# Optimization experiments

Measured on AMD Instinct MI355X. Metric: run time of the kernel, lower is better.

The kernel has to match this reference:

```python
import jax, jax.numpy as jnp
import numpy as np

B, D_IN, H, N_LAYERS, D_OUT = 262144, 8, 128, 3, 1


def setup_inputs() -> dict:
    key = jax.random.key(0)
    ks = jax.random.split(key, 18)
    rn = lambda k, shape, fan: (jax.random.normal(k, shape, jnp.float32) / np.sqrt(fan))
    return {
        "x": jax.random.normal(ks[0], (B, D_IN), jnp.float32),
        "Sw_w": rn(ks[1], (D_IN, H), D_IN),
        "Sw_b": rn(ks[2], (H,), D_IN),
        "Uz": rn(ks[3], (N_LAYERS, D_IN, H), D_IN),
        "Wsz_w": rn(ks[4], (N_LAYERS, H, H), H),
        "Wsz_b": rn(ks[5], (N_LAYERS, H), H),
        "Ug": rn(ks[6], (N_LAYERS, D_IN, H), D_IN),
        "Wsg_w": rn(ks[7], (N_LAYERS, H, H), H),
        "Wsg_b": rn(ks[8], (N_LAYERS, H), H),
        "Ur": rn(ks[9], (N_LAYERS, D_IN, H), D_IN),
        "Wsr_w": rn(ks[10], (N_LAYERS, H, H), H),
        "Wsr_b": rn(ks[11], (N_LAYERS, H), H),
        "Uh": rn(ks[12], (N_LAYERS, D_IN, H), D_IN),
        "Wsh_w": rn(ks[13], (N_LAYERS, H, H), H),
        "Wsh_b": rn(ks[14], (N_LAYERS, H), H),
        "Wf_w": rn(ks[15], (H, D_OUT), H),
        "Wf_b": rn(ks[16], (D_OUT,), H),
    }


def reference(x, Sw_w, Sw_b, Uz, Wsz_w, Wsz_b, Ug, Wsg_w, Wsg_b,
              Ur, Wsr_w, Wsr_b, Uh, Wsh_w, Wsh_b, Wf_w, Wf_b):
    # x: [B, D_in]; S: [B, H]
    S = x @ Sw_w + Sw_b
    n = Uz.shape[0]
    for i in range(n):  # small fixed layer count
        S = jax.nn.sigmoid(S)
        Z = jax.nn.sigmoid(x @ Uz[i] + S @ Wsz_w[i] + Wsz_b[i])
        G = jax.nn.sigmoid(x @ Ug[i] + S @ Wsg_w[i] + Wsg_b[i])
        R = jax.nn.sigmoid(x @ Ur[i] + S @ Wsr_w[i] + Wsr_b[i])
        H_ = jnp.tanh(x @ Uh[i] + (S * R) @ Wsh_w[i] + Wsh_b[i])
        S = (1.0 - G) * H_ + Z * S
    return S @ Wf_w + Wf_b  # [B, D_out]
```

## Files before the change

### kernel.cpp

```cpp
#include <hip/hip_runtime.h>

typedef __bf16 bf16_t;
typedef __bf16 bf16x4 __attribute__((ext_vector_type(4)));
typedef __bf16 bf16x8 __attribute__((ext_vector_type(8)));
typedef float f32x4 __attribute__((ext_vector_type(4)));

#define NL 3
#define HD 128
#define ROWS 64
#define SSTR 136
#define RSTR 136
#define XSTR 24
#define THREADS 512
#define BATCH 262144
#define NBLK (BATCH / ROWS)

#define SW_OFF 0
#define U_OFF  4096
#define W_OFF  53248
#define WS_ELEMS 249856

#define MFMA(a, b, c) __builtin_amdgcn_mfma_f32_16x16x32_bf16((a), (b), (c), 0, 0, 0)

#define LOG2E 1.4426950408889634f
__device__ __forceinline__ float sige(float a) {
    return __builtin_amdgcn_rcpf(1.f + __builtin_amdgcn_exp2f(a));
}
__device__ __forceinline__ float tanhe(float a) {
    return 1.f - 2.f * __builtin_amdgcn_rcpf(__builtin_amdgcn_exp2f(a) + 1.f);
}
__device__ __forceinline__ float sigm(float v) {
    return __builtin_amdgcn_rcpf(1.f + __builtin_amdgcn_exp2f(-LOG2E * v));
}

__global__ void dgm_prep(const float* __restrict__ SwW, const float* __restrict__ Swb,
                         const float* __restrict__ Uz, const float* __restrict__ Wz, const float* __restrict__ Bz,
                         const float* __restrict__ Ug, const float* __restrict__ Wg, const float* __restrict__ Bg,
                         const float* __restrict__ Ur, const float* __restrict__ Wr, const float* __restrict__ Br,
                         const float* __restrict__ Uh, const float* __restrict__ Wh,
                         bf16_t* __restrict__ ws) {
    int idx = blockIdx.x * 256 + threadIdx.x;
    if (idx >= WS_ELEMS) return;
    const float* Us[4] = {Uz, Ug, Ur, Uh};
    const float* Wm[4] = {Wz, Wg, Wr, Wh};
    const float gsc[4] = {-LOG2E, LOG2E, -LOG2E, 2.f * LOG2E};
    if (idx < U_OFF) {
        int ct = idx >> 9, rem = idx & 511, lane = rem >> 3, j = rem & 7;
        int q = lane >> 4, mm = lane & 15;
        int k = q * 8 + j, n = ct * 16 + mm;
        float v = (k < 8) ? SwW[k * HD + n] : (k == 8) ? Swb[n] : 0.f;
        ws[idx] = (bf16_t)(v * -LOG2E);
    } else if (idx < W_OFF) {
        int t = idx - U_OFF;
        int lg = t >> 12, r2 = t & 4095;
        int l = lg >> 2, g = lg & 3;
        int ct = r2 >> 9, rem = r2 & 511, lane = rem >> 3, j = rem & 7;
        int q = lane >> 4, mm = lane & 15;
        int k = q * 8 + j, n = ct * 16 + mm;
        const float* Bs = (g == 0) ? Bz : (g == 1) ? Bg : (g == 2) ? Br : (const float*)0;
        float v = (k < 8) ? Us[g][(l * 8 + k) * HD + n]
                : (k == 8 && g < 3) ? Bs[l * HD + n] : 0.f;
        ws[idx] = (bf16_t)(v * gsc[g]);
    } else {
        int t = idx - W_OFF;
        int lg = t >> 14, r2 = t & 16383;
        int l = lg >> 2, g = lg & 3;
        int ct = r2 >> 11, kc = (r2 >> 9) & 3, rem = r2 & 511, lane = rem >> 3, j = rem & 7;
        int q = lane >> 4, mm = lane & 15;
        int k = kc * 32 + q * 8 + j, n = ct * 16 + mm;
        ws[idx] = (bf16_t)(Wm[g][(l * HD + k) * HD + n] * gsc[g]);
    }
}

__global__ __launch_bounds__(THREADS, 4) void dgm_main(
    const float* __restrict__ x,
    const float* __restrict__ Bh,
    const float* __restrict__ WfW, const float* __restrict__ WfB,
    const bf16_t* __restrict__ ws,
    float* __restrict__ out) {
    __shared__ __align__(16) bf16_t s_sig[ROWS * SSTR];
    __shared__ __align__(16) bf16_t s_r[ROWS * RSTR];
    __shared__ __align__(16) bf16_t s_xo[ROWS * XSTR];
    __shared__ float red[ROWS];

    const int tid = threadIdx.x;
    const int lane = tid & 63;
    const int ct = tid >> 6;
    const int m = lane & 15, q = lane >> 4;
    const int rb = blockIdx.x * ROWS;
    const int f0 = ct * 16 + q * 4;
    const int fragoff = (ct * 64 + lane) * 8;
    const int wfragoff = (ct * 4) * 512 + lane * 8;
    const int xoff = (q ? 8 : 0);

    if (tid < ROWS) red[tid] = 0.f;

    {
        int r = tid >> 3, j = tid & 7;
        s_xo[r * XSTR + j] = (bf16_t)x[(size_t)(rb + r) * 8 + j];
        s_xo[r * XSTR + 8 + j] = (j == 0) ? (bf16_t)1.f : (bf16_t)0.f;
    }
    __syncthreads();

    bf16x4 svp[4];

    {
        bf16x8 fSw = *(const bf16x8*)(ws + SW_OFF + fragoff);
#pragma unroll
        for (int bt = 0; bt < 4; bt++) {
            bf16x8 b = *(const bf16x8*)(&s_xo[(bt * 16 + m) * XSTR + xoff]);
            f32x4 acc = {0.f, 0.f, 0.f, 0.f};
            acc = MFMA(fSw, b, acc);
            bf16x4 pk;
#pragma unroll
            for (int i = 0; i < 4; i++) pk[i] = (bf16_t)sige(acc[i]);
            svp[bt] = pk;
            *(bf16x4*)(&s_sig[(bt * 16 + m) * SSTR + f0]) = pk;
        }
    }
    __syncthreads();

#pragma unroll 1
    for (int l = 0; l < NL; l++) {
        const bool last = (l == NL - 1);
        const bf16_t* wb = ws + W_OFF + (size_t)l * 4 * 16384;
        const bf16_t* ub = ws + U_OFF + (size_t)l * 4 * 4096;

        {
            bf16x8 fU = *(const bf16x8*)(ub + 2 * 4096 + fragoff);
            bf16x8 fW[4];
#pragma unroll
            for (int kc = 0; kc < 4; kc++)
                fW[kc] = *(const bf16x8*)(wb + 2 * 16384 + wfragoff + kc * 512);
#pragma unroll
            for (int bt = 0; bt < 4; bt++) {
                const bf16_t* bbase = &s_sig[(bt * 16 + m) * SSTR];
                const bf16_t* xbase = &s_xo[(bt * 16 + m) * XSTR];
                f32x4 aR = {0.f, 0.f, 0.f, 0.f};
#pragma unroll
                for (int kc = 0; kc < 4; kc++) {
                    bf16x8 b = *(const bf16x8*)(bbase + kc * 32 + q * 8);
                    aR = MFMA(fW[kc], b, aR);
                }
                {
                    bf16x8 b = *(const bf16x8*)(xbase + xoff);
                    aR = MFMA(fU, b, aR);
                }
                bf16x4 pk;
#pragma unroll
                for (int i = 0; i < 4; i++)
                    pk[i] = (bf16_t)(sige(aR[i]) * (float)svp[bt][i]);
                *(bf16x4*)(&s_r[(bt * 16 + m) * RSTR + f0]) = pk;
            }
        }

        bf16x4 t1p[4];
        bf16x4 ogp[4];

        {
            bf16x8 fUz = *(const bf16x8*)(ub + 0 * 4096 + fragoff);
            bf16x8 fUg = *(const bf16x8*)(ub + 1 * 4096 + fragoff);
            bf16x8 fWz[4], fWg[4];
#pragma unroll
            for (int kc = 0; kc < 4; kc++) {
                fWz[kc] = *(const bf16x8*)(wb + 0 * 16384 + wfragoff + kc * 512);
                fWg[kc] = *(const bf16x8*)(wb + 1 * 16384 + wfragoff + kc * 512);
            }
#pragma unroll
            for (int bt = 0; bt < 4; bt++) {
                const bf16_t* bbase = &s_sig[(bt * 16 + m) * SSTR];
                const bf16_t* xbase = &s_xo[(bt * 16 + m) * XSTR];
                f32x4 aZ = {0.f, 0.f, 0.f, 0.f}, aG = {0.f, 0.f, 0.f, 0.f};
#pragma unroll
                for (int kc = 0; kc < 4; kc++) {
                    bf16x8 b = *(const bf16x8*)(bbase + kc * 32 + q * 8);
                    aZ = MFMA(fWz[kc], b, aZ);
                    aG = MFMA(fWg[kc], b, aG);
                }
                {
                    bf16x8 b = *(const bf16x8*)(xbase + xoff);
                    aZ = MFMA(fUz, b, aZ);
                    aG = MFMA(fUg, b, aG);
                }
                bf16x4 t1, og;
#pragma unroll
                for (int i = 0; i < 4; i++) {
                    t1[i] = (bf16_t)(sige(aZ[i]) * (float)svp[bt][i]);
                    og[i] = (bf16_t)sige(aG[i]);
                }
                t1p[bt] = t1;
                ogp[bt] = og;
            }
        }
        __syncthreads();

        {
            bf16x8 fU = *(const bf16x8*)(ub + 3 * 4096 + fragoff);
            bf16x8 fW[4];
#pragma unroll
            for (int kc = 0; kc < 4; kc++)
                fW[kc] = *(const bf16x8*)(wb + 3 * 16384 + wfragoff + kc * 512);
            f32x4 bh4 = *(const f32x4*)&Bh[l * HD + f0];
#pragma unroll
            for (int i = 0; i < 4; i++) bh4[i] *= 2.f * LOG2E;
#pragma unroll
            for (int bt = 0; bt < 4; bt++) {
                const bf16_t* bbase = &s_r[(bt * 16 + m) * RSTR];
                const bf16_t* xbase = &s_xo[(bt * 16 + m) * XSTR];
                f32x4 aH = {0.f, 0.f, 0.f, 0.f};
#pragma unroll
                for (int kc = 0; kc < 4; kc++) {
                    bf16x8 b = *(const bf16x8*)(bbase + kc * 32 + q * 8);
                    aH = MFMA(fW[kc], b, aH);
                }
                {
                    bf16x8 b = *(const bf16x8*)(xbase);
                    aH = MFMA(fU, b, aH);
                }
                if (last) {
                    const f32x4 wf4 = *(const f32x4*)&WfW[f0];
                    float p = 0.f;
#pragma unroll
                    for (int i = 0; i < 4; i++) {
                        float hh = tanhe(aH[i] + bh4[i]);
                        float sn = (float)ogp[bt][i] * hh + (float)t1p[bt][i];
                        p += sn * wf4[i];
                    }
                    p += __shfl_xor(p, 16);
                    p += __shfl_xor(p, 32);
                    if (q == 0) atomicAdd(&red[bt * 16 + m], p);
                } else {
                    bf16x4 pk;
#pragma unroll
                    for (int i = 0; i < 4; i++) {
                        float hh = tanhe(aH[i] + bh4[i]);
                        float sn = (float)ogp[bt][i] * hh + (float)t1p[bt][i];
                        pk[i] = (bf16_t)sigm(sn);
                    }
                    svp[bt] = pk;
                    *(bf16x4*)(&s_sig[(bt * 16 + m) * SSTR + f0]) = pk;
                }
            }
        }
        __syncthreads();
    }

    if (tid < ROWS) out[rb + tid] = red[tid] + WfB[0];
}

extern "C" void kernel_launch(void* const* d_in, const int* in_sizes, int n_in,
                              void* d_out, int out_size, void* d_ws, size_t ws_size,
                              hipStream_t stream) {
    const float* x   = (const float*)d_in[0];
    const float* SwW = (const float*)d_in[1];
    const float* Swb = (const float*)d_in[2];
    const float* Uz  = (const float*)d_in[3];
    const float* Wz  = (const float*)d_in[4];
    const float* Bz  = (const float*)d_in[5];
    const float* Ug  = (const float*)d_in[6];
    const float* Wg  = (const float*)d_in[7];
    const float* Bg  = (const float*)d_in[8];
    const float* Ur  = (const float*)d_in[9];
    const float* Wr  = (const float*)d_in[10];
    const float* Br  = (const float*)d_in[11];
    const float* Uh  = (const float*)d_in[12];
    const float* Wh  = (const float*)d_in[13];
    const float* Bh  = (const float*)d_in[14];
    const float* WfW = (const float*)d_in[15];
    const float* WfB = (const float*)d_in[16];
    bf16_t* ws = (bf16_t*)d_ws;
    float* out = (float*)d_out;

    if (ws_size < (size_t)WS_ELEMS * sizeof(bf16_t)) return;

    dgm_prep<<<(WS_ELEMS + 255) / 256, 256, 0, stream>>>(SwW, Swb, Uz, Wz, Bz, Ug, Wg, Bg,
                                                         Ur, Wr, Br, Uh, Wh, ws);
    dgm_main<<<NBLK, THREADS, 0, stream>>>(x, Bh, WfW, WfB, ws, out);
}
```

Baseline: 264.2 us.

## Fold H-gate bias into U fragment, split Z/G passes, raise occupancy bound

Folds the Bh bias into the bf16 U-fragment of the H gate through the ones-column of x, so the per-layer bias load and scale disappear from the main loop. The fused Z/G MFMA pass becomes two sequential passes, each holding only one gate's weight fragments, and the WfW load is hoisted out of the batch-tile loop. Together with raising launch_bounds min blocks from 4 to 5, the aim is to lower register pressure and fit more waves per CU. The costs are re-reading the s_sig/x fragments from LDS twice, less MFMA interleaving, and Bh rounded to bf16.

Result: slower. 301.9 us (+14.3%).

```diff
diff --git a/kernel.cpp b/kernel.cpp
--- a/kernel.cpp
+++ b/kernel.cpp
@@ -37,7 +37,7 @@
                          const float* __restrict__ Uz, const float* __restrict__ Wz, const float* __restrict__ Bz,
                          const float* __restrict__ Ug, const float* __restrict__ Wg, const float* __restrict__ Bg,
                          const float* __restrict__ Ur, const float* __restrict__ Wr, const float* __restrict__ Br,
-                         const float* __restrict__ Uh, const float* __restrict__ Wh,
+                         const float* __restrict__ Uh, const float* __restrict__ Wh, const float* __restrict__ Bh,
                          bf16_t* __restrict__ ws) {
     int idx = blockIdx.x * 256 + threadIdx.x;
     if (idx >= WS_ELEMS) return;
@@ -57,9 +57,9 @@
         int ct = r2 >> 9, rem = r2 & 511, lane = rem >> 3, j = rem & 7;
         int q = lane >> 4, mm = lane & 15;
         int k = q * 8 + j, n = ct * 16 + mm;
-        const float* Bs = (g == 0) ? Bz : (g == 1) ? Bg : (g == 2) ? Br : (const float*)0;
+        const float* Bs = (g == 0) ? Bz : (g == 1) ? Bg : (g == 2) ? Br : Bh;
         float v = (k < 8) ? Us[g][(l * 8 + k) * HD + n]
-                : (k == 8 && g < 3) ? Bs[l * HD + n] : 0.f;
+                : (k == 8) ? Bs[l * HD + n] : 0.f;
         ws[idx] = (bf16_t)(v * gsc[g]);
     } else {
         int t = idx - W_OFF;
@@ -72,7 +72,7 @@
     }
 }
 
-__global__ __launch_bounds__(THREADS, 4) void dgm_main(
+__global__ __launch_bounds__(THREADS, 5) void dgm_main(
     const float* __restrict__ x,
     const float* __restrict__ Bh,
     const float* __restrict__ WfW, const float* __restrict__ WfB,
@@ -158,37 +158,57 @@
         bf16x4 ogp[4];
 
         {
-            bf16x8 fUz = *(const bf16x8*)(ub + 0 * 4096 + fragoff);
-            bf16x8 fUg = *(const bf16x8*)(ub + 1 * 4096 + fragoff);
-            bf16x8 fWz[4], fWg[4];
-#pragma unroll
-            for (int kc = 0; kc < 4; kc++) {
-                fWz[kc] = *(const bf16x8*)(wb + 0 * 16384 + wfragoff + kc * 512);
-                fWg[kc] = *(const bf16x8*)(wb + 1 * 16384 + wfragoff + kc * 512);
-            }
+            bf16x8 fU = *(const bf16x8*)(ub + 0 * 4096 + fragoff);
+            bf16x8 fW[4];
+#pragma unroll
+            for (int kc = 0; kc < 4; kc++)
+                fW[kc] = *(const bf16x8*)(wb + 0 * 16384 + wfragoff + kc * 512);
 #pragma unroll
             for (int bt = 0; bt < 4; bt++) {
                 const bf16_t* bbase = &s_sig[(bt * 16 + m) * SSTR];
                 const bf16_t* xbase = &s_xo[(bt * 16 + m) * XSTR];
-                f32x4 aZ = {0.f, 0.f, 0.f, 0.f}, aG = {0.f, 0.f, 0.f, 0.f};
-#pragma unroll
-                for (int kc = 0; kc < 4; kc++) {
-                    bf16x8 b = *(const bf16x8*)(bbase + kc * 32 + q * 8);
-                    aZ = MFMA(fWz[kc], b, aZ);
-                    aG = MFMA(fWg[kc], b, aG);
-                }
-                {
-                    bf16x8 b = *(const bf16x8*)(xbase + xoff);
-                    aZ = MFMA(fUz, b, aZ);
-                    aG = MFMA(fUg, b, aG);
-                }
-                bf16x4 t1, og;
-#pragma unroll
-                for (int i = 0; i < 4; i++) {
+                f32x4 aZ = {0.f, 0.f, 0.f, 0.f};
+#pragma unroll
+                for (int kc = 0; kc < 4; kc++) {
+                    bf16x8 b = *(const bf16x8*)(bbase + kc * 32 + q * 8);
+                    aZ = MFMA(fW[kc], b, aZ);
+                }
+                {
+                    bf16x8 b = *(const bf16x8*)(xbase + xoff);
+                    aZ = MFMA(fU, b, aZ);
+                }
+                bf16x4 t1;
+#pragma unroll
+                for (int i = 0; i < 4; i++)
                     t1[i] = (bf16_t)(sige(aZ[i]) * (float)svp[bt][i]);
+                t1p[bt] = t1;
+            }
+        }
+
+        {
+            bf16x8 fU = *(const bf16x8*)(ub + 1 * 4096 + fragoff);
+            bf16x8 fW[4];
+#pragma unroll
+            for (int kc = 0; kc < 4; kc++)
+                fW[kc] = *(const bf16x8*)(wb + 1 * 16384 + wfragoff + kc * 512);
+#pragma unroll
+            for (int bt = 0; bt < 4; bt++) {
+                const bf16_t* bbase = &s_sig[(bt * 16 + m) * SSTR];
+                const bf16_t* xbase = &s_xo[(bt * 16 + m) * XSTR];
+                f32x4 aG = {0.f, 0.f, 0.f, 0.f};
+#pragma unroll
+                for (int kc = 0; kc < 4; kc++) {
+                    bf16x8 b = *(const bf16x8*)(bbase + kc * 32 + q * 8);
+                    aG = MFMA(fW[kc], b, aG);
+                }
+                {
+                    bf16x8 b = *(const bf16x8*)(xbase + xoff);
+                    aG = MFMA(fU, b, aG);
+                }
+                bf16x4 og;
+#pragma unroll
+                for (int i = 0; i < 4; i++)
                     og[i] = (bf16_t)sige(aG[i]);
-                }
-                t1p[bt] = t1;
                 ogp[bt] = og;
             }
         }
@@ -200,9 +220,8 @@
 #pragma unroll
             for (int kc = 0; kc < 4; kc++)
                 fW[kc] = *(const bf16x8*)(wb + 3 * 16384 + wfragoff + kc * 512);
-            f32x4 bh4 = *(const f32x4*)&Bh[l * HD + f0];
-#pragma unroll
-            for (int i = 0; i < 4; i++) bh4[i] *= 2.f * LOG2E;
+            f32x4 wf4;
+            if (last) wf4 = *(const f32x4*)&WfW[f0];
 #pragma unroll
             for (int bt = 0; bt < 4; bt++) {
                 const bf16_t* bbase = &s_r[(bt * 16 + m) * RSTR];
@@ -214,15 +233,14 @@
                     aH = MFMA(fW[kc], b, aH);
                 }
                 {
-                    bf16x8 b = *(const bf16x8*)(xbase);
+                    bf16x8 b = *(const bf16x8*)(xbase + xoff);
                     aH = MFMA(fU, b, aH);
                 }
                 if (last) {
-                    const f32x4 wf4 = *(const f32x4*)&WfW[f0];
                     float p = 0.f;
 #pragma unroll
                     for (int i = 0; i < 4; i++) {
-                        float hh = tanhe(aH[i] + bh4[i]);
+                        float hh = tanhe(aH[i]);
                         float sn = (float)ogp[bt][i] * hh + (float)t1p[bt][i];
                         p += sn * wf4[i];
                     }
@@ -233,7 +251,7 @@
                     bf16x4 pk;
 #pragma unroll
                     for (int i = 0; i < 4; i++) {
-                        float hh = tanhe(aH[i] + bh4[i]);
+                        float hh = tanhe(aH[i]);
                         float sn = (float)ogp[bt][i] * hh + (float)t1p[bt][i];
                         pk[i] = (bf16_t)sigm(sn);
                     }
@@ -274,6 +292,6 @@
     if (ws_size < (size_t)WS_ELEMS * sizeof(bf16_t)) return;
 
     dgm_prep<<<(WS_ELEMS + 255) / 256, 256, 0, stream>>>(SwW, Swb, Uz, Wz, Bz, Ug, Wg, Bg,
-                                                         Ur, Wr, Br, Uh, Wh, ws);
+                                                         Ur, Wr, Br, Uh, Wh, Bh, ws);
     dgm_main<<<NBLK, THREADS, 0, stream>>>(x, Bh, WfW, WfB, ws, out);
 }
```
